# Kernel optimization log

Measured on AMD Instinct MI355X. Metric: run time of the kernel, lower is better.

## Reference

```python
import jax, jax.numpy as jnp
import numpy as np

NEG_SLOPE = 0.2


def _gat_layer(x, src, dst, n, W, a_src, a_dst, b, concat):
    """PyG-style GATConv (inference, self-loops already in src/dst).
    x: [N, Fin]; W: [Fin, H*C]; a_src/a_dst: [H, C]; b: [H*C] or [C]."""
    H, C = a_src.shape
    h = (x @ W).reshape(-1, H, C)                      # [N, H, C]
    al_s = jnp.einsum('nhc,hc->nh', h, a_src)          # [N, H]
    al_d = jnp.einsum('nhc,hc->nh', h, a_dst)          # [N, H]
    e = al_s[src] + al_d[dst]                          # [E, H]
    e = jnp.where(e >= 0, e, NEG_SLOPE * e)            # LeakyReLU(0.2)
    m = jax.ops.segment_max(e, dst, num_segments=n)    # [N, H] softmax over dst
    e = jnp.exp(e - m[dst])
    s = jax.ops.segment_sum(e, dst, num_segments=n)    # [N, H]
    alpha = e / (s[dst] + 1e-16)                       # [E, H]
    msg = h[src] * alpha[:, :, None]                   # [E, H, C]
    out = jax.ops.segment_sum(msg, dst, num_segments=n)  # [N, H, C]
    if concat:
        out = out.reshape(-1, H * C)
    else:
        out = out.mean(axis=1)
    return out + b


def _forward(x, edge_index, W1, as1, ad1, b1, W2, as2, ad2, b2, W3, as3, ad3, b3):
    n = x.shape[0]
    loops = jnp.arange(n, dtype=edge_index.dtype)
    src = jnp.concatenate([edge_index[0], loops])      # add self-loops (PyG default)
    dst = jnp.concatenate([edge_index[1], loops])
    x = _gat_layer(x, src, dst, n, W1, as1, ad1, b1, concat=True)
    x = jax.nn.elu(x)
    x = _gat_layer(x, src, dst, n, W2, as2, ad2, b2, concat=True)
    x = jax.nn.elu(x)
    x = _gat_layer(x, src, dst, n, W3, as3, ad3, b3, concat=False)
    return x


def setup_inputs() -> dict:
    key = jax.random.key(0)
    ks = jax.random.split(key, 16)
    N, E, FIN, HID, H, OUT = 50000, 320000, 256, 64, 4, 64
    sc = 0.1  # keep attention logits in a sane range
    return {
        'x': jax.random.normal(ks[0], (N, FIN), jnp.float32),
        'edge_index': jax.random.randint(ks[1], (2, E), 0, N, jnp.int32),
        'W1': jax.random.normal(ks[2], (FIN, H * HID), jnp.float32) * sc,
        'as1': jax.random.normal(ks[3], (H, HID), jnp.float32) * sc,
        'ad1': jax.random.normal(ks[4], (H, HID), jnp.float32) * sc,
        'b1': jax.random.normal(ks[5], (H * HID,), jnp.float32) * sc,
        'W2': jax.random.normal(ks[6], (H * HID, H * HID), jnp.float32) * sc,
        'as2': jax.random.normal(ks[7], (H, HID), jnp.float32) * sc,
        'ad2': jax.random.normal(ks[8], (H, HID), jnp.float32) * sc,
        'b2': jax.random.normal(ks[9], (H * HID,), jnp.float32) * sc,
        'W3': jax.random.normal(ks[10], (H * HID, OUT), jnp.float32) * sc,
        'as3': jax.random.normal(ks[11], (1, OUT), jnp.float32) * sc,
        'ad3': jax.random.normal(ks[12], (1, OUT), jnp.float32) * sc,
        'b3': jax.random.normal(ks[13], (OUT,), jnp.float32) * sc,
    }


def reference(x, edge_index, W1, as1, ad1, b1, W2, as2, ad2, b2, W3, as3, ad3, b3):
    return _forward(x, edge_index, W1, as1, ad1, b1, W2, as2, ad2, b2, W3, as3, ad3, b3)
```

## Files before the change

### kernel.cpp

```cpp
#include <hip/hip_runtime.h>


typedef __attribute__((ext_vector_type(8))) __bf16 bf16x8;
typedef __attribute__((ext_vector_type(4))) float f32x4;
typedef _Float16 f16x8 __attribute__((ext_vector_type(8)));
typedef _Float16 f16x4 __attribute__((ext_vector_type(4)));

#define NEG_SLOPE 0.2f
#define WELL 40

__device__ __forceinline__ unsigned short f2b_rne(float f) {
    unsigned int u = __float_as_uint(f);
    u += 0x7FFFu + ((u >> 16) & 1u);
    return (unsigned short)(u >> 16);
}
__device__ __forceinline__ unsigned short f2h(float f) {
    _Float16 h = (_Float16)f;
    unsigned short s;
    __builtin_memcpy(&s, &h, 2);
    return s;
}
__device__ __forceinline__ bf16x8 cvt8(const float* f) {
    unsigned short r[8];
#pragma unroll
    for (int j = 0; j < 8; j++) r[j] = f2b_rne(f[j]);
    bf16x8 v;
    __builtin_memcpy(&v, r, 16);
    return v;
}
__device__ __forceinline__ float lrelu(float e) {
    return e >= 0.f ? e : NEG_SLOPE * e;
}

__global__ __launch_bounds__(256) void k_init(const float* __restrict__ W1,
                                              const float* __restrict__ W2,
                                              const float* __restrict__ W3,
                                              unsigned short* __restrict__ W1t,
                                              unsigned short* __restrict__ W2t,
                                              unsigned short* __restrict__ W3t,
                                              int* __restrict__ cnt, int n) {
    int t = blockIdx.x * blockDim.x + threadIdx.x;
    if (t < n) cnt[t] = 0;
    const float* W;
    unsigned short* Wt;
    int Nout, idx = t;
    if (idx < 65536)        { W = W1; Wt = W1t; Nout = 256; }
    else if (idx < 131072)  { W = W2; Wt = W2t; Nout = 256; idx -= 65536; }
    else if (idx < 147456)  { W = W3; Wt = W3t; Nout = 64;  idx -= 131072; }
    else return;
    int k = idx / Nout;
    int c = idx - k * Nout;
    Wt[(size_t)c * 256 + k] = f2b_rne(W[idx]);
}

template <int NT, bool AF32, bool FILL>
__global__ __launch_bounds__(512) void k_gemm(const void* __restrict__ Av,
                                              const __bf16* __restrict__ Bt,
                                              unsigned short* __restrict__ h16,
                                              float* __restrict__ als,
                                              float* __restrict__ ald,
                                              const float* __restrict__ a_s,
                                              const float* __restrict__ a_d,
                                              int M, int H,
                                              const int* __restrict__ esrc,
                                              const int* __restrict__ edst,
                                              int* __restrict__ cnt,
                                              int* __restrict__ ell,
                                              int E, int mtiles) {
    constexpr int NN = NT * 16;
    __shared__ __align__(16) __bf16 Bs[NN][256];

    if (FILL && (int)blockIdx.x >= mtiles) {
        int t = ((int)blockIdx.x - mtiles) * (int)blockDim.x + (int)threadIdx.x;
        int stride = ((int)gridDim.x - mtiles) * (int)blockDim.x;
        for (; t < E; t += stride) {
            int d = edst[t];
            int pos = atomicAdd(&cnt[d], 1);
            if (pos < WELL) ell[(size_t)d * WELL + pos] = esrc[t];
        }
        return;
    }

    const int tid = threadIdx.x;
    const int lane = tid & 63;
    const int w = tid >> 6;
    const int i = lane & 15;
    const int quad = lane >> 4;
    const int m0 = blockIdx.x * 256;

    {
        int nl = lane >> 5;
        int p = lane & 31;
#pragma unroll
        for (int t = 0; t < NN / 16; t++) {
            int n = t * 16 + w * 2 + nl;
            int g = p ^ (n & 7);
            const __bf16* gp = Bt + (size_t)n * 256 + g * 8;
            __builtin_amdgcn_global_load_lds(
                (const __attribute__((address_space(1))) void*)gp,
                (__attribute__((address_space(3))) void*)&Bs[t * 16 + w * 2][0],
                16, 0, 0);
        }
    }

    int ra = m0 + w * 32 + i;
    int rb = ra + 16;
    if (ra >= M) ra = M - 1;
    if (rb >= M) rb = M - 1;

    bf16x8 afrag[2][8];
    if (AF32) {
        const float* pa = (const float*)Av + (size_t)ra * 256;
        const float* pb = (const float*)Av + (size_t)rb * 256;
#pragma unroll
        for (int half = 0; half < 2; half++) {
            float tmp[2][4][8];
#pragma unroll
            for (int k4 = 0; k4 < 4; k4++) {
                int koff = (half * 4 + k4) * 32 + quad * 8;
                *(float4*)&tmp[0][k4][0] = *(const float4*)(pa + koff);
                *(float4*)&tmp[0][k4][4] = *(const float4*)(pa + koff + 4);
                *(float4*)&tmp[1][k4][0] = *(const float4*)(pb + koff);
                *(float4*)&tmp[1][k4][4] = *(const float4*)(pb + koff + 4);
            }
#pragma unroll
            for (int k4 = 0; k4 < 4; k4++) {
                afrag[0][half * 4 + k4] = cvt8(tmp[0][k4]);
                afrag[1][half * 4 + k4] = cvt8(tmp[1][k4]);
            }
        }
    } else {
        const __bf16* pa = (const __bf16*)Av + (size_t)ra * 256;
        const __bf16* pb = (const __bf16*)Av + (size_t)rb * 256;
#pragma unroll
        for (int kc = 0; kc < 8; kc++) {
            int koff = kc * 32 + quad * 8;
            afrag[0][kc] = *(const bf16x8*)(pa + koff);
            afrag[1][kc] = *(const bf16x8*)(pb + koff);
        }
    }

    f32x4 acc[2][NT] = {};

    __syncthreads();

#pragma unroll
    for (int kc = 0; kc < 8; kc++) {
        const int c = kc * 4 + quad;
#pragma unroll
        for (int nt = 0; nt < NT; nt++) {
            const int n = nt * 16 + i;
            const int p = c ^ (n & 7);
            bf16x8 bfv = *(const bf16x8*)&Bs[n][p * 8];
            acc[0][nt] = __builtin_amdgcn_mfma_f32_16x16x32_bf16(
                afrag[0][kc], bfv, acc[0][nt], 0, 0, 0);
            acc[1][nt] = __builtin_amdgcn_mfma_f32_16x16x32_bf16(
                afrag[1][kc], bfv, acc[1][nt], 0, 0, 0);
        }
    }

    float asv[NT], adv[NT];
#pragma unroll
    for (int nt = 0; nt < NT; nt++) {
        asv[nt] = a_s[(nt / 4) * 64 + (nt & 3) * 16 + i];
        adv[nt] = a_d[(nt / 4) * 64 + (nt & 3) * 16 + i];
    }

#pragma unroll
    for (int mt = 0; mt < 2; mt++) {
#pragma unroll
        for (int r = 0; r < 4; r++) {
            int row = m0 + w * 32 + mt * 16 + quad * 4 + r;
            bool ok = row < M;
#pragma unroll
            for (int nt = 0; nt < NT; nt++) {
                if (ok) h16[(size_t)row * NN + nt * 16 + i] = f2h(acc[mt][nt][r]);
            }
#pragma unroll
            for (int g = 0; g < (NT + 3) / 4; g++) {
                float ps = 0.f, pd = 0.f;
#pragma unroll
                for (int j = 0; j < 4 && g * 4 + j < NT; j++) {
                    float v = acc[mt][g * 4 + j][r];
                    ps += v * asv[g * 4 + j];
                    pd += v * adv[g * 4 + j];
                }
#pragma unroll
                for (int off = 1; off <= 8; off <<= 1) {
                    ps += __shfl_xor(ps, off, 64);
                    pd += __shfl_xor(pd, off, 64);
                }
                if (ok && i == 0) {
                    als[(size_t)row * H + g] = ps;
                    ald[(size_t)row * H + g] = pd;
                }
            }
        }
    }
}

__global__ __launch_bounds__(256) void k_agg4(const unsigned short* __restrict__ h16,
                                              const float* __restrict__ als,
                                              const float* __restrict__ ald,
                                              const int* __restrict__ cnt,
                                              const int* __restrict__ ell,
                                              const float* __restrict__ bias,
                                              unsigned short* __restrict__ xout,
                                              int n) {
    int gw = (blockIdx.x * blockDim.x + threadIdx.x) >> 6;
    int lane = threadIdx.x & 63;
    int wid = gw * 2 + (lane >> 5);
    if (wid >= n) return;
    int l = lane & 31;
    int head = l >> 3;
    int ch = l * 8;
    int base = lane & 32;

    int deg = min(cnt[wid], WELL);
    const int* row = ell + (size_t)wid * WELL;
    int myid = (l < deg) ? row[l] : 0;

    float aldv = ald[wid * 4 + head];
    float p = __expf(fminf(lrelu(als[wid * 4 + head] + aldv), 60.f));
    float ssum = p;
    float a[8];
    {
        f16x8 h0 = *(const f16x8*)&h16[(size_t)wid * 256 + ch];
#pragma unroll
        for (int j = 0; j < 8; j++) a[j] = p * (float)h0[j];
    }

    int jmax = min(deg, 32);
    int dm1 = deg - 1;
    for (int j = 0; j < jmax; j += 4) {
        int s0 = __shfl(myid, base + min(j, dm1));
        int s1 = __shfl(myid, base + min(j + 1, dm1));
        int s2 = __shfl(myid, base + min(j + 2, dm1));
        int s3 = __shfl(myid, base + min(j + 3, dm1));
        float e0 = als[s0 * 4 + head];
        float e1 = als[s1 * 4 + head];
        float e2 = als[s2 * 4 + head];
        float e3 = als[s3 * 4 + head];
        f16x8 v0 = *(const f16x8*)&h16[(size_t)s0 * 256 + ch];
        f16x8 v1 = *(const f16x8*)&h16[(size_t)s1 * 256 + ch];
        f16x8 v2 = *(const f16x8*)&h16[(size_t)s2 * 256 + ch];
        f16x8 v3 = *(const f16x8*)&h16[(size_t)s3 * 256 + ch];
        float p0 = __expf(fminf(lrelu(e0 + aldv), 60.f));
        float p1 = (j + 1 < deg) ? __expf(fminf(lrelu(e1 + aldv), 60.f)) : 0.f;
        float p2 = (j + 2 < deg) ? __expf(fminf(lrelu(e2 + aldv), 60.f)) : 0.f;
        float p3 = (j + 3 < deg) ? __expf(fminf(lrelu(e3 + aldv), 60.f)) : 0.f;
        ssum += (p0 + p1) + (p2 + p3);
#pragma unroll
        for (int k = 0; k < 8; k++) {
            a[k] += (p0 * (float)v0[k] + p1 * (float)v1[k]) +
                    (p2 * (float)v2[k] + p3 * (float)v3[k]);
        }
    }
    for (int j = 32; j < deg; ++j) {
        int s0 = row[j];
        float p0 = __expf(fminf(lrelu(als[s0 * 4 + head] + aldv), 60.f));
        f16x8 v0 = *(const f16x8*)&h16[(size_t)s0 * 256 + ch];
        ssum += p0;
#pragma unroll
        for (int k = 0; k < 8; k++) a[k] += p0 * (float)v0[k];
    }

    float inv = 1.f / (ssum + 1e-16f);
    float bb[8];
    *(float4*)&bb[0] = *(const float4*)&bias[ch];
    *(float4*)&bb[4] = *(const float4*)&bias[ch + 4];
    unsigned short o[8];
#pragma unroll
    for (int k = 0; k < 8; k++) {
        float r = a[k] * inv + bb[k];
        r = r > 0.f ? r : expm1f(r);
        o[k] = f2b_rne(r);
    }
    *(int4*)&xout[(size_t)wid * 256 + ch] = *(const int4*)&o[0];
}

__global__ __launch_bounds__(256) void k_agg1(const unsigned short* __restrict__ h16,
                                              const float* __restrict__ als,
                                              const float* __restrict__ ald,
                                              const int* __restrict__ cnt,
                                              const int* __restrict__ ell,
                                              const float* __restrict__ bias,
                                              float* __restrict__ out, int n) {
    int gw = (blockIdx.x * blockDim.x + threadIdx.x) >> 6;
    int lane = threadIdx.x & 63;
    int wid = gw * 8 + (lane >> 3);
    if (wid >= n) return;
    int l = lane & 7;
    int ch = l * 8;
    int base = lane & 56;

    int deg = min(cnt[wid], WELL);
    const int* row = ell + (size_t)wid * WELL;
    int myid = (l < deg) ? row[l] : 0;

    float aldv = ald[wid];
    float p = __expf(fminf(lrelu(als[wid] + aldv), 60.f));
    float ssum = p;
    float a[8];
    {
        f16x8 hv = *(const f16x8*)&h16[(size_t)wid * 64 + ch];
#pragma unroll
        for (int k = 0; k < 8; k++) a[k] = p * (float)hv[k];
    }

    int dm1 = deg - 1;
    for (int j = 0; j < deg; j += 4) {
        int i0 = min(j, dm1), i1 = min(j + 1, dm1);
        int i2 = min(j + 2, dm1), i3 = min(j + 3, dm1);
        int s0, s1, s2, s3;
        if (j < 8) {
            s0 = __shfl(myid, base + i0);
            s1 = __shfl(myid, base + i1);
            s2 = __shfl(myid, base + i2);
            s3 = __shfl(myid, base + i3);
        } else {
            s0 = row[i0]; s1 = row[i1]; s2 = row[i2]; s3 = row[i3];
        }
        float e0 = als[s0], e1 = als[s1], e2 = als[s2], e3 = als[s3];
        f16x8 v0 = *(const f16x8*)&h16[(size_t)s0 * 64 + ch];
        f16x8 v1 = *(const f16x8*)&h16[(size_t)s1 * 64 + ch];
        f16x8 v2 = *(const f16x8*)&h16[(size_t)s2 * 64 + ch];
        f16x8 v3 = *(const f16x8*)&h16[(size_t)s3 * 64 + ch];
        float p0 = __expf(fminf(lrelu(e0 + aldv), 60.f));
        float p1 = (j + 1 < deg) ? __expf(fminf(lrelu(e1 + aldv), 60.f)) : 0.f;
        float p2 = (j + 2 < deg) ? __expf(fminf(lrelu(e2 + aldv), 60.f)) : 0.f;
        float p3 = (j + 3 < deg) ? __expf(fminf(lrelu(e3 + aldv), 60.f)) : 0.f;
        ssum += (p0 + p1) + (p2 + p3);
#pragma unroll
        for (int k = 0; k < 8; k++)
            a[k] += (p0 * (float)v0[k] + p1 * (float)v1[k]) +
                    (p2 * (float)v2[k] + p3 * (float)v3[k]);
    }

    float inv = 1.f / (ssum + 1e-16f);
    float bb[8];
    *(float4*)&bb[0] = *(const float4*)&bias[ch];
    *(float4*)&bb[4] = *(const float4*)&bias[ch + 4];
    float r[8];
#pragma unroll
    for (int k = 0; k < 8; k++) r[k] = a[k] * inv + bb[k];
    *(float4*)&out[(size_t)wid * 64 + ch] = *(const float4*)&r[0];
    *(float4*)&out[(size_t)wid * 64 + ch + 4] = *(const float4*)&r[4];
}

extern "C" void kernel_launch(void* const* d_in, const int* in_sizes, int n_in,
                              void* d_out, int out_size, void* d_ws, size_t ws_size,
                              hipStream_t stream) {
    const float* x   = (const float*)d_in[0];
    const int*   ei  = (const int*)d_in[1];
    const float* W1  = (const float*)d_in[2];
    const float* as1 = (const float*)d_in[3];
    const float* ad1 = (const float*)d_in[4];
    const float* b1  = (const float*)d_in[5];
    const float* W2  = (const float*)d_in[6];
    const float* as2 = (const float*)d_in[7];
    const float* ad2 = (const float*)d_in[8];
    const float* b2  = (const float*)d_in[9];
    const float* W3  = (const float*)d_in[10];
    const float* as3 = (const float*)d_in[11];
    const float* ad3 = (const float*)d_in[12];
    const float* b3  = (const float*)d_in[13];

    const int N = in_sizes[0] / 256;
    const int E = in_sizes[1] / 2;

    size_t off = 0;
    auto alloc = [&](size_t bytes) -> void* {
        void* p = (char*)d_ws + off;
        off += (bytes + 255) & ~(size_t)255;
        return p;
    };
    unsigned short* xb  = (unsigned short*)alloc((size_t)N * 256 * 2);
    unsigned short* W1t = (unsigned short*)alloc((size_t)256 * 256 * 2);
    unsigned short* W2t = (unsigned short*)alloc((size_t)256 * 256 * 2);
    unsigned short* W3t = (unsigned short*)alloc((size_t)64 * 256 * 2);
    unsigned short* h16 = (unsigned short*)alloc((size_t)N * 256 * 2);
    float* als = (float*)alloc((size_t)N * 4 * 4);
    float* ald = (float*)alloc((size_t)N * 4 * 4);
    int* cnt   = (int*)alloc((size_t)N * 4);
    int* ell   = (int*)alloc((size_t)N * WELL * 4);

    const int T = 256;
    const int agg4_blocks = (N + 7) / 8;
    const int agg1_blocks = (N + 31) / 32;
    const int mtiles = (N + 255) / 256;

    k_init<<<dim3(576), T, 0, stream>>>(W1, W2, W3, W1t, W2t, W3t, cnt, N);

    k_gemm<16, true, true><<<dim3(mtiles + 60), 512, 0, stream>>>(
        x, (const __bf16*)W1t, h16, als, ald, as1, ad1, N, 4,
        ei, ei + E, cnt, ell, E, mtiles);
    k_agg4<<<dim3(agg4_blocks), T, 0, stream>>>(h16, als, ald, cnt, ell, b1, xb, N);

    k_gemm<16, false, false><<<dim3(mtiles), 512, 0, stream>>>(
        xb, (const __bf16*)W2t, h16, als, ald, as2, ad2, N, 4,
        nullptr, nullptr, nullptr, nullptr, 0, mtiles);
    k_agg4<<<dim3(agg4_blocks), T, 0, stream>>>(h16, als, ald, cnt, ell, b2, xb, N);

    k_gemm<4, false, false><<<dim3(mtiles), 512, 0, stream>>>(
        xb, (const __bf16*)W3t, h16, als, ald, as3, ad3, N, 1,
        nullptr, nullptr, nullptr, nullptr, 0, mtiles);
    k_agg1<<<dim3(agg1_blocks), T, 0, stream>>>(h16, als, ald, cnt, ell, b3,
                                                (float*)d_out, N);
}
```

Measured before the change: 253.6 us.

## Restructure GEMM into 64-row tiles with K-chunked LDS staging of weights

The GEMM kernel now uses 256-thread blocks, each covering 64 rows instead of 256, and stages the transposed weight matrix into shared memory in four 64-wide K chunks rather than loading the full 256-wide K slice at once. This shrinks LDS use from 128KB to 32KB per block so more blocks fit per CU, and the next chunk's A-operand is prefetched while MFMAs run on the current one. The cost is more barriers per block, four times as many blocks each reloading the full weight matrix, and less A-row reuse per wave.

```diff
diff --git a/kernel.cpp b/kernel.cpp
--- a/kernel.cpp
+++ b/kernel.cpp
@@ -54,7 +54,7 @@
 }
 
 template <int NT, bool AF32, bool FILL>
-__global__ __launch_bounds__(512) void k_gemm(const void* __restrict__ Av,
+__global__ __launch_bounds__(256, 4) void k_gemm(const void* __restrict__ Av,
                                               const __bf16* __restrict__ Bt,
                                               unsigned short* __restrict__ h16,
                                               float* __restrict__ als,
@@ -66,13 +66,13 @@
                                               const int* __restrict__ edst,
                                               int* __restrict__ cnt,
                                               int* __restrict__ ell,
-                                              int E, int mtiles) {
+                                              int E, int gblocks) {
     constexpr int NN = NT * 16;
-    __shared__ __align__(16) __bf16 Bs[NN][256];
-
-    if (FILL && (int)blockIdx.x >= mtiles) {
-        int t = ((int)blockIdx.x - mtiles) * (int)blockDim.x + (int)threadIdx.x;
-        int stride = ((int)gridDim.x - mtiles) * (int)blockDim.x;
+    __shared__ __align__(16) __bf16 Bs[NN][64];
+
+    if (FILL && (int)blockIdx.x >= gblocks) {
+        int t = ((int)blockIdx.x - gblocks) * (int)blockDim.x + (int)threadIdx.x;
+        int stride = ((int)gridDim.x - gblocks) * (int)blockDim.x;
         for (; t < E; t += stride) {
             int d = edst[t];
             int pos = atomicAdd(&cnt[d], 1);
@@ -86,114 +86,128 @@
     const int w = tid >> 6;
     const int i = lane & 15;
     const int quad = lane >> 4;
-    const int m0 = blockIdx.x * 256;
-
-    {
-        int nl = lane >> 5;
-        int p = lane & 31;
-#pragma unroll
-        for (int t = 0; t < NN / 16; t++) {
-            int n = t * 16 + w * 2 + nl;
-            int g = p ^ (n & 7);
-            const __bf16* gp = Bt + (size_t)n * 256 + g * 8;
+    const int m0 = (int)blockIdx.x * 64;
+
+    const int st_r = (lane >> 3);
+    const int st_p = lane & 7;
+    auto stage = [&](int q) {
+#pragma unroll
+        for (int t = 0; t < NN / 32; t++) {
+            int rowbase = t * 32 + w * 8;
+            int r = rowbase + st_r;
+            int c = st_p ^ (r & 7);
+            const __bf16* gp = Bt + (size_t)r * 256 + q * 64 + c * 8;
             __builtin_amdgcn_global_load_lds(
                 (const __attribute__((address_space(1))) void*)gp,
-                (__attribute__((address_space(3))) void*)&Bs[t * 16 + w * 2][0],
+                (__attribute__((address_space(3))) void*)&Bs[rowbase][0],
                 16, 0, 0);
         }
-    }
-
-    int ra = m0 + w * 32 + i;
-    int rb = ra + 16;
+    };
+
+    int ra = m0 + w * 16 + i;
     if (ra >= M) ra = M - 1;
-    if (rb >= M) rb = M - 1;
-
-    bf16x8 afrag[2][8];
+
+    f32x4 acc[NT] = {};
+    bf16x8 afc[2];
+
+    stage(0);
+    float t0[2][8];
     if (AF32) {
         const float* pa = (const float*)Av + (size_t)ra * 256;
-        const float* pb = (const float*)Av + (size_t)rb * 256;
-#pragma unroll
-        for (int half = 0; half < 2; half++) {
-            float tmp[2][4][8];
-#pragma unroll
-            for (int k4 = 0; k4 < 4; k4++) {
-                int koff = (half * 4 + k4) * 32 + quad * 8;
-                *(float4*)&tmp[0][k4][0] = *(const float4*)(pa + koff);
-                *(float4*)&tmp[0][k4][4] = *(const float4*)(pa + koff + 4);
-                *(float4*)&tmp[1][k4][0] = *(const float4*)(pb + koff);
-                *(float4*)&tmp[1][k4][4] = *(const float4*)(pb + koff + 4);
-            }
-#pragma unroll
-            for (int k4 = 0; k4 < 4; k4++) {
-                afrag[0][half * 4 + k4] = cvt8(tmp[0][k4]);
-                afrag[1][half * 4 + k4] = cvt8(tmp[1][k4]);
-            }
+#pragma unroll
+        for (int kc2 = 0; kc2 < 2; kc2++) {
+            int koff = kc2 * 32 + quad * 8;
+            *(float4*)&t0[kc2][0] = *(const float4*)(pa + koff);
+            *(float4*)&t0[kc2][4] = *(const float4*)(pa + koff + 4);
         }
     } else {
         const __bf16* pa = (const __bf16*)Av + (size_t)ra * 256;
-        const __bf16* pb = (const __bf16*)Av + (size_t)rb * 256;
-#pragma unroll
-        for (int kc = 0; kc < 8; kc++) {
-            int koff = kc * 32 + quad * 8;
-            afrag[0][kc] = *(const bf16x8*)(pa + koff);
-            afrag[1][kc] = *(const bf16x8*)(pb + koff);
-        }
-    }
-
-    f32x4 acc[2][NT] = {};
-
+        afc[0] = *(const bf16x8*)(pa + quad * 8);
+        afc[1] = *(const bf16x8*)(pa + 32 + quad * 8);
+    }
     __syncthreads();
-
-#pragma unroll
-    for (int kc = 0; kc < 8; kc++) {
-        const int c = kc * 4 + quad;
+    if (AF32) {
+        afc[0] = cvt8(t0[0]);
+        afc[1] = cvt8(t0[1]);
+    }
+
+#pragma unroll
+    for (int q = 0; q < 4; q++) {
+        float tn[2][8];
+        bf16x8 afn[2];
+        if (q < 3) {
+            if (AF32) {
+                const float* pa = (const float*)Av + (size_t)ra * 256 + (q + 1) * 64;
+#pragma unroll
+                for (int kc2 = 0; kc2 < 2; kc2++) {
+                    int koff = kc2 * 32 + quad * 8;
+                    *(float4*)&tn[kc2][0] = *(const float4*)(pa + koff);
+                    *(float4*)&tn[kc2][4] = *(const float4*)(pa + koff + 4);
+                }
+            } else {
+                const __bf16* pa = (const __bf16*)Av + (size_t)ra * 256 + (q + 1) * 64;
+                afn[0] = *(const bf16x8*)(pa + quad * 8);
+                afn[1] = *(const bf16x8*)(pa + 32 + quad * 8);
+            }
+        }
+#pragma unroll
+        for (int kc2 = 0; kc2 < 2; kc2++) {
+            const int c = kc2 * 4 + quad;
+#pragma unroll
+            for (int nt = 0; nt < NT; nt++) {
+                const int n = nt * 16 + i;
+                const int p = c ^ (n & 7);
+                bf16x8 bfv = *(const bf16x8*)&Bs[n][p * 8];
+                acc[nt] = __builtin_amdgcn_mfma_f32_16x16x32_bf16(
+                    afc[kc2], bfv, acc[nt], 0, 0, 0);
+            }
+        }
+        if (q < 3) {
+            if (AF32) {
+                afc[0] = cvt8(tn[0]);
+                afc[1] = cvt8(tn[1]);
+            } else {
+                afc[0] = afn[0];
+                afc[1] = afn[1];
+            }
+            __syncthreads();
+            stage(q + 1);
+            __syncthreads();
+        }
+    }
+
+    float asv[NT], adv[NT];
+#pragma unroll
+    for (int nt = 0; nt < NT; nt++) {
+        asv[nt] = a_s[(nt >> 2) * 64 + (nt & 3) * 16 + i];
+        adv[nt] = a_d[(nt >> 2) * 64 + (nt & 3) * 16 + i];
+    }
+
+#pragma unroll
+    for (int r = 0; r < 4; r++) {
+        int row = m0 + w * 16 + quad * 4 + r;
+        bool ok = row < M;
 #pragma unroll
         for (int nt = 0; nt < NT; nt++) {
-            const int n = nt * 16 + i;
-            const int p = c ^ (n & 7);
-            bf16x8 bfv = *(const bf16x8*)&Bs[n][p * 8];
-            acc[0][nt] = __builtin_amdgcn_mfma_f32_16x16x32_bf16(
-                afrag[0][kc], bfv, acc[0][nt], 0, 0, 0);
-            acc[1][nt] = __builtin_amdgcn_mfma_f32_16x16x32_bf16(
-                afrag[1][kc], bfv, acc[1][nt], 0, 0, 0);
-        }
-    }
-
-    float asv[NT], adv[NT];
-#pragma unroll
-    for (int nt = 0; nt < NT; nt++) {
-        asv[nt] = a_s[(nt / 4) * 64 + (nt & 3) * 16 + i];
-        adv[nt] = a_d[(nt / 4) * 64 + (nt & 3) * 16 + i];
-    }
-
-#pragma unroll
-    for (int mt = 0; mt < 2; mt++) {
-#pragma unroll
-        for (int r = 0; r < 4; r++) {
-            int row = m0 + w * 32 + mt * 16 + quad * 4 + r;
-            bool ok = row < M;
-#pragma unroll
-            for (int nt = 0; nt < NT; nt++) {
-                if (ok) h16[(size_t)row * NN + nt * 16 + i] = f2h(acc[mt][nt][r]);
-            }
-#pragma unroll
-            for (int g = 0; g < (NT + 3) / 4; g++) {
-                float ps = 0.f, pd = 0.f;
-#pragma unroll
-                for (int j = 0; j < 4 && g * 4 + j < NT; j++) {
-                    float v = acc[mt][g * 4 + j][r];
-                    ps += v * asv[g * 4 + j];
-                    pd += v * adv[g * 4 + j];
-                }
-#pragma unroll
-                for (int off = 1; off <= 8; off <<= 1) {
-                    ps += __shfl_xor(ps, off, 64);
-                    pd += __shfl_xor(pd, off, 64);
-                }
-                if (ok && i == 0) {
-                    als[(size_t)row * H + g] = ps;
-                    ald[(size_t)row * H + g] = pd;
-                }
+            if (ok) h16[(size_t)row * NN + nt * 16 + i] = f2h(acc[nt][r]);
+        }
+#pragma unroll
+        for (int g = 0; g < (NT + 3) / 4; g++) {
+            float ps = 0.f, pd = 0.f;
+#pragma unroll
+            for (int j = 0; j < 4 && g * 4 + j < NT; j++) {
+                float v = acc[g * 4 + j][r];
+                ps += v * asv[g * 4 + j];
+                pd += v * adv[g * 4 + j];
+            }
+#pragma unroll
+            for (int off = 1; off <= 8; off <<= 1) {
+                ps += __shfl_xor(ps, off, 64);
+                pd += __shfl_xor(pd, off, 64);
+            }
+            if (ok && i == 0) {
+                als[(size_t)row * H + g] = ps;
+                ald[(size_t)row * H + g] = pd;
             }
         }
     }
@@ -388,21 +402,21 @@
     const int T = 256;
     const int agg4_blocks = (N + 7) / 8;
     const int agg1_blocks = (N + 31) / 32;
-    const int mtiles = (N + 255) / 256;
+    const int mtiles = (N + 63) / 64;
 
     k_init<<<dim3(576), T, 0, stream>>>(W1, W2, W3, W1t, W2t, W3t, cnt, N);
 
-    k_gemm<16, true, true><<<dim3(mtiles + 60), 512, 0, stream>>>(
+    k_gemm<16, true, true><<<dim3(mtiles + 60), T, 0, stream>>>(
         x, (const __bf16*)W1t, h16, als, ald, as1, ad1, N, 4,
         ei, ei + E, cnt, ell, E, mtiles);
     k_agg4<<<dim3(agg4_blocks), T, 0, stream>>>(h16, als, ald, cnt, ell, b1, xb, N);
 
-    k_gemm<16, false, false><<<dim3(mtiles), 512, 0, stream>>>(
+    k_gemm<16, false, false><<<dim3(mtiles), T, 0, stream>>>(
         xb, (const __bf16*)W2t, h16, als, ald, as2, ad2, N, 4,
         nullptr, nullptr, nullptr, nullptr, 0, mtiles);
     k_agg4<<<dim3(agg4_blocks), T, 0, stream>>>(h16, als, ald, cnt, ell, b2, xb, N);
 
-    k_gemm<4, false, false><<<dim3(mtiles), 512, 0, stream>>>(
+    k_gemm<4, false, false><<<dim3(mtiles), T, 0, stream>>>(
         xb, (const __bf16*)W3t, h16, als, ald, as3, ad3, N, 1,
         nullptr, nullptr, nullptr, nullptr, 0, mtiles);
     k_agg1<<<dim3(agg1_blocks), T, 0, stream>>>(h16, als, ald, cnt, ell, b3,
```

Result: slower. 263.7 us (+4.0%).
